# Kernel tuning notes

Hardware: AMD Instinct MI355X
Metric: run time of the kernel (lower is better)

The kernel has to match this reference:

```python
import jax, jax.numpy as jnp
import numpy as np
from jax import lax

# Quantized ConvBnA block: int8 conv with int32 accumulation, per-channel
# bias add (folded BN), power-of-two requant via arithmetic right shift,
# clamp, and narrow-int cast (uint8 since Act_min >= 0 -> pure_positive).

N, CIN, COUT, H, W, K = 32, 128, 256, 56, 56, 3

def setup_inputs() -> dict:
    key = jax.random.key(0)
    k1, k2, k3 = jax.random.split(key, 3)
    # int8-valued inputs / weights (stored as int32 per harness dtype support)
    x = jax.random.randint(k1, (N, CIN, H, W), -64, 64, dtype=jnp.int32)
    weight = jax.random.randint(k2, (COUT, CIN, K, K), -128, 128, dtype=jnp.int32)
    # BN_shift is negative (shift right by -n = 8 bits)
    n = jnp.full((1, COUT, 1, 1), -8, dtype=jnp.int32)
    # folded-BN integer bias, broadcasts over [N, C, H, W]
    t = jax.random.randint(k3, (1, COUT, 1, 1), -2048, 2048, dtype=jnp.int32)
    act_min = 0
    act_max = 255
    return {"x": x, "weight": weight, "n": n, "t": t,
            "act_min": act_min, "act_max": act_max}

def reference(x, weight, n, t, act_min, act_max):
    # int32-accumulated convolution (stride 1, pad 1, dilation 1, groups 1)
    acc = lax.conv_general_dilated(
        x.astype(jnp.int32), weight.astype(jnp.int32),
        window_strides=(1, 1), padding=((1, 1), (1, 1)),
        dimension_numbers=("NCHW", "OIHW", "NCHW"))
    acc = acc + t                              # folded-BN bias add
    acc = jnp.right_shift(acc, -n)             # pow2 requant, arithmetic shift
    acc = jnp.clip(acc, jnp.int32(act_min), jnp.int32(act_max))
    # pure_positive (Act_min >= 0) -> small unsigned type
    return acc.astype(jnp.uint8)
```

## Files before the change

### kernel.cpp

```cpp
#include <hip/hip_runtime.h>
#include <cstdint>


typedef __attribute__((ext_vector_type(4))) int i32x4;
typedef __attribute__((ext_vector_type(2))) int i32x2;

#define C_IN   128
#define HW2    3136
#define OUT_NSTRIDE 802816

#define XQ_BYTES 12845056
#define WQ_OFF   XQ_BYTES
#define WQ_BYTES 294912
#define ZP_OFF   (WQ_OFF + WQ_BYTES)

__device__ __forceinline__ void gload_lds16(const void* g, void* l) {
  __builtin_amdgcn_global_load_lds(
      (const __attribute__((address_space(1))) void*)(uintptr_t)g,
      (__attribute__((address_space(3))) void*)(uint32_t)(uintptr_t)l,
      16, 0, 0);
}

__global__ void wxform(const int* __restrict__ w, char* __restrict__ wq,
                       int* __restrict__ zp) {
  int id = blockIdx.x * 256 + threadIdx.x;
  int ci = id & 127;
  int co = (id >> 7) & 255;
  int g  = id >> 15;
  wq[id] = (char)w[co * 1152 + ci * 9 + g];
  if (blockIdx.x == 0 && threadIdx.x < 64) zp[threadIdx.x] = 0;
}

__global__ __launch_bounds__(256) void xform(const int* __restrict__ x,
                                             char* __restrict__ xq) {
  int bid = blockIdx.x;
  int hb = bid % 49;
  int n  = bid / 49;
  int t  = threadIdx.x;
  int cig = t & 15;
  int hw0 = (t >> 4) * 4;
  const int* src = x + n * (C_IN * HW2) + hb * 64 + hw0;
  i32x4 ld[8];
#pragma unroll
  for (int j = 0; j < 8; j++)
    ld[j] = *(const i32x4*)(src + (cig * 8 + j) * HW2);
  char* dst = xq + (size_t)(n * HW2 + hb * 64 + hw0) * 128 + cig * 8;
#pragma unroll
  for (int p = 0; p < 4; p++) {
    unsigned lo = (ld[0][p] & 255) | ((ld[1][p] & 255) << 8) |
                  ((ld[2][p] & 255) << 16) | ((unsigned)(ld[3][p] & 255) << 24);
    unsigned hi = (ld[4][p] & 255) | ((ld[5][p] & 255) << 8) |
                  ((ld[6][p] & 255) << 16) | ((unsigned)(ld[7][p] & 255) << 24);
    i32x2 v; v[0] = (int)lo; v[1] = (int)hi;
    *(i32x2*)(dst + p * 128) = v;
  }
}

__global__ __launch_bounds__(512, 1) void conv_mfma(
    const char* __restrict__ xq, const char* __restrict__ wq,
    const char* __restrict__ zp,
    const int* __restrict__ nshift, const int* __restrict__ tbias,
    const int* __restrict__ aminp, const int* __restrict__ amaxp,
    int* __restrict__ out) {
  __shared__ char lds[98304];

  const int tid = threadIdx.x;
  const int bid = blockIdx.x;
  const int swz = (bid & 7) * 196 + (bid >> 3);
  const int bm = swz / 784;
  const int pb = swz % 784;
  const int l   = tid & 63;
  const int wid = tid >> 6;
  const int wm = wid >> 2;
  const int wn = wid & 3;

  const int r_ = tid & 127;
  const int c0 = tid >> 7;
  const char* wsrcA = wq + (bm * 128 + r_) * 128;
  const int p = pb * 128 + r_;
  const int n_img = p / HW2;
  const int hw = p - n_img * HW2;
  const int ph = hw / 56, pw = hw - (hw / 56) * 56;
  const char* xsrc = xq + (size_t)p * 128;

  auto stageA = [&](int g, char* Ab) {
    const char* s = wsrcA + g * 32768;
    gload_lds16(s + c0 * 16,       Ab + (c0 * 128 + r_) * 16);
    gload_lds16(s + (c0 + 4) * 16, Ab + ((c0 + 4) * 128 + r_) * 16);
  };
  auto stageB = [&](int g, char* Bb) {
    const int g3 = g / 3;
    const int dh = g3 - 1, dw = g - g3 * 3 - 1;
    const bool valid = ((unsigned)(ph + dh) < 56u) && ((unsigned)(pw + dw) < 56u);
    const char* s = valid ? (xsrc + (dh * 56 + dw) * 128) : zp;
    gload_lds16(s + c0 * 16,       Bb + (c0 * 128 + r_) * 16);
    gload_lds16(s + (c0 + 4) * 16, Bb + ((c0 + 4) * 128 + r_) * 16);
  };

  i32x4 acc[4][2] = {};
  const int lrow16 = (l & 15) * 16;
  const int lch = l >> 4;

  stageA(0, lds);            stageB(0, lds + 16384);
  stageA(1, lds + 32768);    stageB(1, lds + 32768 + 16384);

  int cur = 0;
#pragma unroll 1
  for (int t = 0; t < 9; ++t) {
    if (t < 8) { asm volatile("s_waitcnt vmcnt(4)" ::: "memory"); }
    else       { asm volatile("s_waitcnt vmcnt(0)" ::: "memory"); }
    __builtin_amdgcn_s_barrier();

    char* Ab = lds + cur * 32768;
    char* Bb = Ab + 16384;
    int nxt = cur + 2; if (nxt >= 3) nxt -= 3;
    char* An = lds + nxt * 32768;

#pragma unroll
    for (int kk = 0; kk < 2; ++kk) {
      i32x4 a[4], b[2];
      const int coff = (kk * 4 + lch) * 2048;
#pragma unroll
      for (int mi = 0; mi < 4; mi++)
        a[mi] = *(const i32x4*)(Ab + coff + wm * 1024 + mi * 256 + lrow16);
#pragma unroll
      for (int ni = 0; ni < 2; ni++)
        b[ni] = *(const i32x4*)(Bb + coff + wn * 512 + ni * 256 + lrow16);
      if (t < 7) {
        if (kk == 0) stageA(t + 2, An);
        else         stageB(t + 2, An + 16384);
      }
      __builtin_amdgcn_s_barrier();
      asm volatile("s_waitcnt lgkmcnt(0)" ::: "memory");
      __builtin_amdgcn_sched_barrier(0);
      __builtin_amdgcn_s_setprio(1);
#pragma unroll
      for (int mi = 0; mi < 4; mi++)
#pragma unroll
        for (int ni = 0; ni < 2; ni++)
          acc[mi][ni] = __builtin_amdgcn_mfma_i32_16x16x64_i8(
              a[mi], b[ni], acc[mi][ni], 0, 0, 0);
      __builtin_amdgcn_s_setprio(0);
      __builtin_amdgcn_sched_barrier(0);
      __builtin_amdgcn_s_barrier();
    }
    cur = cur + 1; if (cur == 3) cur = 0;
  }

  const int amin = aminp[0], amax = amaxp[0];
  int pbase[2];
#pragma unroll
  for (int ni = 0; ni < 2; ni++) {
    int pp = pb * 128 + wn * 32 + ni * 16 + (l & 15);
    int nn = pp / HW2;
    int hh = pp - nn * HW2;
    pbase[ni] = nn * OUT_NSTRIDE + hh;
  }
#pragma unroll
  for (int mi = 0; mi < 4; mi++) {
    int co0 = bm * 128 + wm * 64 + mi * 16 + ((l >> 4) << 2);
    const int4 t4 = *(const int4*)(tbias + co0);
    const int4 n4 = *(const int4*)(nshift + co0);
#pragma unroll
    for (int ni = 0; ni < 2; ni++) {
#pragma unroll
      for (int r = 0; r < 4; r++) {
        int tv = (r == 0) ? t4.x : (r == 1) ? t4.y : (r == 2) ? t4.z : t4.w;
        int nv = (r == 0) ? n4.x : (r == 1) ? n4.y : (r == 2) ? n4.z : n4.w;
        int v = acc[mi][ni][r] + tv;
        v = v >> (-nv);
        v = v < amin ? amin : (v > amax ? amax : v);
        out[pbase[ni] + (co0 + r) * HW2] = v;
      }
    }
  }
}

extern "C" void kernel_launch(void* const* d_in, const int* in_sizes, int n_in,
                              void* d_out, int out_size, void* d_ws, size_t ws_size,
                              hipStream_t stream) {
  const int* x      = (const int*)d_in[0];
  const int* w      = (const int*)d_in[1];
  const int* nshift = (const int*)d_in[2];
  const int* tbias  = (const int*)d_in[3];
  const int* aminp  = (const int*)d_in[4];
  const int* amaxp  = (const int*)d_in[5];
  int* out = (int*)d_out;

  char* xq = (char*)d_ws;
  char* wq = (char*)d_ws + WQ_OFF;
  char* zp = (char*)d_ws + ZP_OFF;

  hipLaunchKernelGGL(wxform, dim3(1152), dim3(256), 0, stream, w, wq, (int*)zp);
  hipLaunchKernelGGL(xform,  dim3(1568), dim3(256), 0, stream, x, xq);
  hipLaunchKernelGGL(conv_mfma, dim3(1568), dim3(512), 0, stream,
                     xq, wq, zp, nshift, tbias, aminp, amaxp, out);
}
```

Before: 215.6 us.

## Shrink conv block to 4 waves with 64x64 warp tiles and halved K-stage

```diff
diff --git a/kernel.cpp b/kernel.cpp
--- a/kernel.cpp
+++ b/kernel.cpp
@@ -56,13 +56,13 @@
   }
 }
 
-__global__ __launch_bounds__(512, 1) void conv_mfma(
+__global__ __launch_bounds__(256, 3) void conv_mfma(
     const char* __restrict__ xq, const char* __restrict__ wq,
     const char* __restrict__ zp,
     const int* __restrict__ nshift, const int* __restrict__ tbias,
     const int* __restrict__ aminp, const int* __restrict__ amaxp,
     int* __restrict__ out) {
-  __shared__ char lds[98304];
+  __shared__ char lds[49152];
 
   const int tid = threadIdx.x;
   const int bid = blockIdx.x;
@@ -71,98 +71,82 @@
   const int pb = swz % 784;
   const int l   = tid & 63;
   const int wid = tid >> 6;
-  const int wm = wid >> 2;
-  const int wn = wid & 3;
+  const int wm = wid >> 1, wn = wid & 1;
 
   const int r_ = tid & 127;
-  const int c0 = tid >> 7;
-  const char* wsrcA = wq + (bm * 128 + r_) * 128;
+  const int cA = tid >> 7;
+  const char* wbase = wq + (bm * 128 + r_) * 128;
   const int p = pb * 128 + r_;
   const int n_img = p / HW2;
   const int hw = p - n_img * HW2;
-  const int ph = hw / 56, pw = hw - (hw / 56) * 56;
-  const char* xsrc = xq + (size_t)p * 128;
+  const int ph = hw / 56, pw = hw - ph * 56;
+  const char* xbase = xq + (size_t)p * 128;
 
-  auto stageA = [&](int g, char* Ab) {
-    const char* s = wsrcA + g * 32768;
-    gload_lds16(s + c0 * 16,       Ab + (c0 * 128 + r_) * 16);
-    gload_lds16(s + (c0 + 4) * 16, Ab + ((c0 + 4) * 128 + r_) * 16);
-  };
-  auto stageB = [&](int g, char* Bb) {
+  auto stage = [&](int s, char* buf) {
+    const int g = s >> 1, kh = s & 1;
+    char* Ab = buf;
+    char* Bb = buf + 8192;
+    const char* as = wbase + g * 32768 + kh * 64;
+    gload_lds16(as + cA * 16,       Ab + (cA * 128 + r_) * 16);
+    gload_lds16(as + (cA + 2) * 16, Ab + ((cA + 2) * 128 + r_) * 16);
     const int g3 = g / 3;
     const int dh = g3 - 1, dw = g - g3 * 3 - 1;
     const bool valid = ((unsigned)(ph + dh) < 56u) && ((unsigned)(pw + dw) < 56u);
-    const char* s = valid ? (xsrc + (dh * 56 + dw) * 128) : zp;
-    gload_lds16(s + c0 * 16,       Bb + (c0 * 128 + r_) * 16);
-    gload_lds16(s + (c0 + 4) * 16, Bb + ((c0 + 4) * 128 + r_) * 16);
+    const char* bs = valid ? (xbase + (dh * 56 + dw) * 128 + kh * 64) : zp;
+    gload_lds16(bs + cA * 16,       Bb + (cA * 128 + r_) * 16);
+    gload_lds16(bs + (cA + 2) * 16, Bb + ((cA + 2) * 128 + r_) * 16);
   };
 
-  i32x4 acc[4][2] = {};
-  const int lrow16 = (l & 15) * 16;
-  const int lch = l >> 4;
+  i32x4 acc[4][4] = {};
+  const int lr16 = (l & 15) * 16;
+  const int lch  = l >> 4;
 
-  stageA(0, lds);            stageB(0, lds + 16384);
-  stageA(1, lds + 32768);    stageB(1, lds + 32768 + 16384);
+  stage(0, lds);
+  stage(1, lds + 16384);
 
-  int cur = 0;
 #pragma unroll 1
-  for (int t = 0; t < 9; ++t) {
-    if (t < 8) { asm volatile("s_waitcnt vmcnt(4)" ::: "memory"); }
-    else       { asm volatile("s_waitcnt vmcnt(0)" ::: "memory"); }
+  for (int t = 0; t < 18; ++t) {
+    if (t < 17) { asm volatile("s_waitcnt vmcnt(4)" ::: "memory"); }
+    else        { asm volatile("s_waitcnt vmcnt(0)" ::: "memory"); }
     __builtin_amdgcn_s_barrier();
-
-    char* Ab = lds + cur * 32768;
-    char* Bb = Ab + 16384;
-    int nxt = cur + 2; if (nxt >= 3) nxt -= 3;
-    char* An = lds + nxt * 32768;
-
+    __builtin_amdgcn_sched_barrier(0);
+    const int cur = t % 3;
+    char* Ab = lds + cur * 16384;
+    char* Bb = Ab + 8192;
+    if (t < 16) stage(t + 2, lds + ((t + 2) % 3) * 16384);
+    i32x4 a[4], b[4];
 #pragma unroll
-    for (int kk = 0; kk < 2; ++kk) {
-      i32x4 a[4], b[2];
-      const int coff = (kk * 4 + lch) * 2048;
+    for (int mi = 0; mi < 4; mi++)
+      a[mi] = *(const i32x4*)(Ab + (lch * 128 + wm * 64 + mi * 16) * 16 + lr16);
 #pragma unroll
-      for (int mi = 0; mi < 4; mi++)
-        a[mi] = *(const i32x4*)(Ab + coff + wm * 1024 + mi * 256 + lrow16);
+    for (int ni = 0; ni < 4; ni++)
+      b[ni] = *(const i32x4*)(Bb + (lch * 128 + wn * 64 + ni * 16) * 16 + lr16);
+    __builtin_amdgcn_s_setprio(1);
 #pragma unroll
-      for (int ni = 0; ni < 2; ni++)
-        b[ni] = *(const i32x4*)(Bb + coff + wn * 512 + ni * 256 + lrow16);
-      if (t < 7) {
-        if (kk == 0) stageA(t + 2, An);
-        else         stageB(t + 2, An + 16384);
-      }
-      __builtin_amdgcn_s_barrier();
-      asm volatile("s_waitcnt lgkmcnt(0)" ::: "memory");
-      __builtin_amdgcn_sched_barrier(0);
-      __builtin_amdgcn_s_setprio(1);
+    for (int mi = 0; mi < 4; mi++)
 #pragma unroll
-      for (int mi = 0; mi < 4; mi++)
-#pragma unroll
-        for (int ni = 0; ni < 2; ni++)
-          acc[mi][ni] = __builtin_amdgcn_mfma_i32_16x16x64_i8(
-              a[mi], b[ni], acc[mi][ni], 0, 0, 0);
-      __builtin_amdgcn_s_setprio(0);
-      __builtin_amdgcn_sched_barrier(0);
-      __builtin_amdgcn_s_barrier();
-    }
-    cur = cur + 1; if (cur == 3) cur = 0;
+      for (int ni = 0; ni < 4; ni++)
+        acc[mi][ni] = __builtin_amdgcn_mfma_i32_16x16x64_i8(
+            a[mi], b[ni], acc[mi][ni], 0, 0, 0);
+    __builtin_amdgcn_s_setprio(0);
   }
 
   const int amin = aminp[0], amax = amaxp[0];
-  int pbase[2];
+  int pbase[4];
 #pragma unroll
-  for (int ni = 0; ni < 2; ni++) {
-    int pp = pb * 128 + wn * 32 + ni * 16 + (l & 15);
+  for (int ni = 0; ni < 4; ni++) {
+    int pp = pb * 128 + wn * 64 + ni * 16 + (l & 15);
     int nn = pp / HW2;
     int hh = pp - nn * HW2;
     pbase[ni] = nn * OUT_NSTRIDE + hh;
   }
 #pragma unroll
   for (int mi = 0; mi < 4; mi++) {
-    int co0 = bm * 128 + wm * 64 + mi * 16 + ((l >> 4) << 2);
+    int co0 = bm * 128 + wm * 64 + mi * 16 + (lch << 2);
     const int4 t4 = *(const int4*)(tbias + co0);
     const int4 n4 = *(const int4*)(nshift + co0);
 #pragma unroll
-    for (int ni = 0; ni < 2; ni++) {
+    for (int ni = 0; ni < 4; ni++) {
 #pragma unroll
       for (int r = 0; r < 4; r++) {
         int tv = (r == 0) ? t4.x : (r == 1) ? t4.y : (r == 2) ? t4.z : t4.w;
@@ -193,6 +177,6 @@
 
   hipLaunchKernelGGL(wxform, dim3(1152), dim3(256), 0, stream, w, wq, (int*)zp);
   hipLaunchKernelGGL(xform,  dim3(1568), dim3(256), 0, stream, x, xq);
-  hipLaunchKernelGGL(conv_mfma, dim3(1568), dim3(512), 0, stream,
+  hipLaunchKernelGGL(conv_mfma, dim3(1568), dim3(256), 0, stream,
                      xq, wq, zp, nshift, tbias, aminp, amaxp, out);
 }
```

New measurement: 209.5 us. -2.8%, faster.
